# Kernel optimization log

Measured on AMD Instinct MI355X. Metric: run time of the kernel, lower is better.

## Reference

```python
import jax, jax.numpy as jnp
import numpy as np


def setup_inputs() -> dict:
    key = jax.random.key(0)
    k1, k2, k3, k4 = jax.random.split(key, 4)
    B, G, C, T = 4, 40, 13, 1024
    return {
        "x": jax.random.normal(k1, (B, G, C, T), dtype=jnp.float32),
        "query_w": jax.random.normal(k2, (C, C), dtype=jnp.float32),
        "key_w": jax.random.normal(k3, (C, C), dtype=jnp.float32),
        "value_w": jax.random.normal(k4, (C, C), dtype=jnp.float32),
    }


def reference(x, query_w, key_w, value_w):
    # x: [B, 40, 13, T] real -> rfft over time -> [B, 40, 13, F] complex
    x_fft = jnp.fft.rfft(x, axis=-1)
    cdt = x_fft.dtype
    wq = query_w.astype(cdt)  # [13,13] complex (zero imag), shared across the 40 groups
    wk = key_w.astype(cdt)
    wv = value_w.astype(cdt)
    xt = jnp.swapaxes(x_fft, -1, -2)  # [B, 40, F, 13]
    q = xt @ wq                       # [B, 40, F, 13]
    k = xt @ wk
    v = xt @ wv
    scores = jnp.abs(q @ jnp.swapaxes(k, -1, -2))     # [B, 40, F, F] real
    attn = jax.nn.softmax(scores, axis=-1).astype(cdt)
    out = (attn @ v)                                   # [B, 40, F, 13]
    out = jnp.swapaxes(out, -1, -2)                    # [B, 40, 13, F]
    return jnp.fft.irfft(out, axis=-1)                 # [B, 40, 13, 2*(F-1)]
```

## Files before the change

### kernel.cpp

```cpp
#include <hip/hip_runtime.h>
#include <math.h>

#define BDIM 4
#define GDIM 40
#define CDIM 13
#define TDIM 1024
#define FDIM 513
#define BG   (BDIM*GDIM)
#define NROW (BG*FDIM)
#define NCHUNK 9
#define TK 64

typedef _Float16 half4 __attribute__((ext_vector_type(4)));
typedef _Float16 half8 __attribute__((ext_vector_type(8)));
typedef float    f32x4 __attribute__((ext_vector_type(4)));

#define MFMA16(a, b, c) __builtin_amdgcn_mfma_f32_16x16x16f16((a), (b), (c), 0, 0, 0)

__device__ __forceinline__ unsigned bitrev10(unsigned x) { return __brev(x) >> 22; }

__global__ void fft_fwd2(const float* __restrict__ x, float2* __restrict__ xf) {
    __shared__ float re[1024], im[1024];
    const int s2 = blockIdx.x;
    const float* x1 = x + (size_t)(2 * s2) * TDIM;
    const float* x2 = x1 + TDIM;
    for (int t = threadIdx.x; t < 1024; t += blockDim.x) {
        unsigned r = bitrev10(t);
        re[r] = x1[t];
        im[r] = x2[t];
    }
    __syncthreads();
    for (int s = 0; s < 10; ++s) {
        int half = 1 << s;
        for (int j = threadIdx.x; j < 512; j += blockDim.x) {
            int grp = j >> s;
            int pos = j & (half - 1);
            int i1 = (grp << (s + 1)) + pos;
            int i2 = i1 + half;
            float ang = -(float)M_PI * (float)pos / (float)half;
            float sw, cw; __sincosf(ang, &sw, &cw);
            float xr = re[i2], xi = im[i2];
            float tr = cw * xr - sw * xi;
            float ti = cw * xi + sw * xr;
            float ur = re[i1], ui = im[i1];
            re[i1] = ur + tr; im[i1] = ui + ti;
            re[i2] = ur - tr; im[i2] = ui - ti;
        }
        __syncthreads();
    }
    const int sigA = 2 * s2, sigB = sigA + 1;
    const int bgA = sigA / CDIM, cA = sigA % CDIM;
    const int bgB = sigB / CDIM, cB = sigB % CDIM;
    for (int f = threadIdx.x; f < FDIM; f += blockDim.x) {
        int fr = (1024 - f) & 1023;
        float zr = re[f], zi = im[f];
        float wr = re[fr], wi = im[fr];
        xf[((size_t)bgA * FDIM + f) * CDIM + cA] =
            make_float2(0.5f * (zr + wr), 0.5f * (zi - wi));
        xf[((size_t)bgB * FDIM + f) * CDIM + cB] =
            make_float2(0.5f * (zi + wi), 0.5f * (wr - zr));
    }
}

__global__ void qkv_kernel(const float2* __restrict__ xf,
                           const float* __restrict__ wq,
                           const float* __restrict__ wk,
                           const float* __restrict__ wv,
                           float2* __restrict__ q,
                           _Float16* __restrict__ KP,
                           _Float16* __restrict__ VT) {
    int gid = blockIdx.x * blockDim.x + threadIdx.x;
    if (gid >= NROW * CDIM) return;
    int r = gid / CDIM;
    int i = gid - r * CDIM;
    const float2* xrow = xf + (size_t)r * CDIM;
    float qr = 0, qi = 0, kr = 0, ki = 0, vr = 0, vi = 0;
#pragma unroll
    for (int c = 0; c < CDIM; ++c) {
        float2 xc = xrow[c];
        float a = wq[c * CDIM + i]; qr += xc.x * a; qi += xc.y * a;
        float b = wk[c * CDIM + i]; kr += xc.x * b; ki += xc.y * b;
        float d = wv[c * CDIM + i]; vr += xc.x * d; vi += xc.y * d;
    }
    q[gid] = make_float2(qr, qi);

    _Float16* krow = KP + (size_t)r * 64;
    _Float16 h0 = (_Float16)kr;
    _Float16 h1 = (_Float16)ki;
    krow[i]      = h0;
    krow[13 + i] = h1;
    krow[32 + i] = (_Float16)(kr - (float)h0);
    krow[45 + i] = (_Float16)(ki - (float)h1);
    if (i == 12) {
        *(unsigned int*)(krow + 26) = 0u;
        *(unsigned int*)(krow + 28) = 0u;
        *(unsigned int*)(krow + 30) = 0u;
        *(unsigned int*)(krow + 58) = 0u;
        *(unsigned int*)(krow + 60) = 0u;
        *(unsigned int*)(krow + 62) = 0u;
    }
    int bg = r / FDIM;
    int f  = r - bg * FDIM;
    VT[((size_t)(bg * 2 + 0) * 16 + i) * 520 + f] = (_Float16)vr;
    VT[((size_t)(bg * 2 + 1) * 16 + i) * 520 + f] = (_Float16)vi;
}

__global__ __launch_bounds__(256, 4) void attn_kernel(const float2* __restrict__ q,
                                                      const _Float16* __restrict__ KP,
                                                      const _Float16* __restrict__ VT,
                                                      float2* __restrict__ outspec) {
    __shared__ __align__(16) _Float16 Klds[TK * 64];
    __shared__ __align__(16) _Float16 VTlds[2 * 16 * 72];

    const int bg    = blockIdx.x / NCHUNK;
    const int chunk = blockIdx.x % NCHUNK;
    const int tid   = threadIdx.x;
    const int w     = tid >> 6;
    const int lane  = tid & 63;
    const int qlane = lane & 15;
    const int g     = lane >> 4;
    const int frow  = chunk * 64 + w * 16 + qlane;
    const bool writer = (frow < FDIM);
    const int f     = writer ? frow : (FDIM - 1);
    const size_t rowbase = (size_t)(bg * FDIM + f) * CDIM;

    half4 uh[2], ul[2], u2h[2], u2l[2];
#pragma unroll
    for (int c01 = 0; c01 < 2; ++c01) {
#pragma unroll
        for (int j = 0; j < 4; ++j) {
            int k = c01 * 16 + 4 * g + j;
            float a = 0.f, b = 0.f;
            if (k < CDIM) {
                float2 t = q[rowbase + k];          a = t.x;  b = t.y;
            } else if (k < 2 * CDIM) {
                float2 t = q[rowbase + (k - CDIM)]; a = -t.y; b = t.x;
            }
            _Float16 ah = (_Float16)a;
            uh[c01][j]  = ah;
            ul[c01][j]  = (_Float16)(a - (float)ah);
            _Float16 bh = (_Float16)b;
            u2h[c01][j] = bh;
            u2l[c01][j] = (_Float16)(b - (float)bh);
        }
    }

    f32x4 o_re = {0.f, 0.f, 0.f, 0.f};
    f32x4 o_im = {0.f, 0.f, 0.f, 0.f};
    float m = -INFINITY, l = 0.f;

    const _Float16* __restrict__ KPg = KP + (size_t)bg * FDIM * 64;
    const _Float16* __restrict__ VTg = VT + (size_t)bg * 2 * 16 * 520;

    for (int t0 = 0; t0 < FDIM; t0 += TK) {
        __syncthreads();
#pragma unroll
        for (int hh = 0; hh < 2; ++hh) {
            int gr  = tid + hh * 256;
            int krw = gr >> 3, gg = gr & 7;
            half8 val;
#pragma unroll
            for (int e = 0; e < 8; ++e) val[e] = (_Float16)0.f;
            int grow = t0 + krw;
            if (grow < FDIM)
                val = *(const half8*)(KPg + (size_t)grow * 64 + gg * 8);
            *(half8*)(Klds + krw * 64 + ((gg ^ (krw & 7)) << 3)) = val;
        }
        {
            int gk = tid & 7, cc = (tid >> 3) & 15, part = tid >> 7;
            int rb = t0 + gk * 8;
            half8 val;
#pragma unroll
            for (int e = 0; e < 8; ++e) val[e] = (_Float16)0.f;
            if (rb < FDIM) {
                val = *(const half8*)(VTg + ((size_t)(part * 16 + cc)) * 520 + rb);
                if (rb + 8 > FDIM) {
#pragma unroll
                    for (int e = 0; e < 8; ++e) if (rb + e >= FDIM) val[e] = (_Float16)0.f;
                }
            }
            *(half8*)(VTlds + (part * 16 + cc) * 72 + gk * 8) = val;
        }
        __syncthreads();

#pragma unroll
        for (int sub = 0; sub < 4; ++sub) {
            const int arow = sub * 16 + qlane;
            const int rx   = arow & 7;
            const _Float16* kr = Klds + arow * 64;
#define KFRAG(h) (*(const half4*)(kr + (((((h) >> 3)) ^ rx) << 3) + ((h) & 7)))
            half4 wh0 = KFRAG(4 * g);
            half4 wh1 = KFRAG(16 + 4 * g);
            half4 wl0 = KFRAG(32 + 4 * g);
            half4 wl1 = KFRAG(48 + 4 * g);
#undef KFRAG
            f32x4 sre = {0.f, 0.f, 0.f, 0.f};
            f32x4 sim = {0.f, 0.f, 0.f, 0.f};
            sre = MFMA16(wh0, uh[0], sre);
            sre = MFMA16(wh1, uh[1], sre);
            sre = MFMA16(wl0, uh[0], sre);
            sre = MFMA16(wl1, uh[1], sre);
            sre = MFMA16(wh0, ul[0], sre);
            sre = MFMA16(wh1, ul[1], sre);
            sre = MFMA16(wl0, ul[0], sre);
            sre = MFMA16(wl1, ul[1], sre);
            sim = MFMA16(wh0, u2h[0], sim);
            sim = MFMA16(wh1, u2h[1], sim);
            sim = MFMA16(wl0, u2h[0], sim);
            sim = MFMA16(wl1, u2h[1], sim);
            sim = MFMA16(wh0, u2l[0], sim);
            sim = MFMA16(wh1, u2l[1], sim);
            sim = MFMA16(wl0, u2l[0], sim);
            sim = MFMA16(wl1, u2l[1], sim);

            float s0 = sqrtf(fmaf(sre[0], sre[0], sim[0] * sim[0]));
            float s1 = sqrtf(fmaf(sre[1], sre[1], sim[1] * sim[1]));
            float s2 = sqrtf(fmaf(sre[2], sre[2], sim[2] * sim[2]));
            float s3 = sqrtf(fmaf(sre[3], sre[3], sim[3] * sim[3]));
            float tmax = fmaxf(fmaxf(s0, s1), fmaxf(s2, s3));
            tmax = fmaxf(tmax, __shfl_xor(tmax, 16));
            tmax = fmaxf(tmax, __shfl_xor(tmax, 32));
            float mnew  = fmaxf(m, tmax);
            float alpha = __expf(m - mnew);
            m = mnew;
            l *= alpha;
            o_re *= alpha;
            o_im *= alpha;
            float p0 = __expf(s0 - m);
            float p1 = __expf(s1 - m);
            float p2 = __expf(s2 - m);
            float p3 = __expf(s3 - m);
            l += (p0 + p1) + (p2 + p3);
            half4 pk;
            pk[0] = (_Float16)p0; pk[1] = (_Float16)p1;
            pk[2] = (_Float16)p2; pk[3] = (_Float16)p3;

            const int voff = sub * 16 + 4 * g;
            half4 vfr = *(const half4*)(VTlds + qlane * 72 + voff);
            half4 vfi = *(const half4*)(VTlds + (16 + qlane) * 72 + voff);
            o_re = MFMA16(vfr, pk, o_re);
            o_im = MFMA16(vfi, pk, o_im);
        }
    }

    l += __shfl_xor(l, 16);
    l += __shfl_xor(l, 32);
    if (writer) {
        float inv = 1.f / l;
#pragma unroll
        for (int j = 0; j < 4; ++j) {
            int c = 4 * g + j;
            if (c < CDIM)
                outspec[((size_t)(bg * CDIM + c)) * FDIM + frow] =
                    make_float2(o_re[j] * inv, o_im[j] * inv);
        }
    }
}

__global__ void fft_inv2(const float2* __restrict__ spec, float* __restrict__ out) {
    __shared__ float re[1024], im[1024];
    const int s2 = blockIdx.x;
    const float2* Y1 = spec + (size_t)(2 * s2) * FDIM;
    const float2* Y2 = Y1 + FDIM;
    for (int t = threadIdx.x; t < 1024; t += blockDim.x) {
        float a, b, c, d;
        if (t <= 512) {
            float2 y1 = Y1[t], y2 = Y2[t];
            bool edge = (t == 0) | (t == 512);
            a = y1.x; b = edge ? 0.f : y1.y;
            c = y2.x; d = edge ? 0.f : y2.y;
        } else {
            float2 y1 = Y1[1024 - t], y2 = Y2[1024 - t];
            a = y1.x; b = -y1.y;
            c = y2.x; d = -y2.y;
        }
        unsigned r = bitrev10(t);
        re[r] = a - d;
        im[r] = b + c;
    }
    __syncthreads();
    for (int s = 0; s < 10; ++s) {
        int half = 1 << s;
        for (int j = threadIdx.x; j < 512; j += blockDim.x) {
            int grp = j >> s;
            int pos = j & (half - 1);
            int i1 = (grp << (s + 1)) + pos;
            int i2 = i1 + half;
            float ang = (float)M_PI * (float)pos / (float)half;
            float sw, cw; __sincosf(ang, &sw, &cw);
            float xr = re[i2], xi = im[i2];
            float tr = cw * xr - sw * xi;
            float ti = cw * xi + sw * xr;
            float ur = re[i1], ui = im[i1];
            re[i1] = ur + tr; im[i1] = ui + ti;
            re[i2] = ur - tr; im[i2] = ui - ti;
        }
        __syncthreads();
    }
    const float scale = 1.0f / 1024.0f;
    float* o1 = out + (size_t)(2 * s2) * TDIM;
    for (int t = threadIdx.x; t < 1024; t += blockDim.x) {
        o1[t]        = re[t] * scale;
        o1[TDIM + t] = im[t] * scale;
    }
}

extern "C" void kernel_launch(void* const* d_in, const int* in_sizes, int n_in,
                              void* d_out, int out_size, void* d_ws, size_t ws_size,
                              hipStream_t stream) {
    const float* x  = (const float*)d_in[0];
    const float* wq = (const float*)d_in[1];
    const float* wk = (const float*)d_in[2];
    const float* wv = (const float*)d_in[3];
    float* out = (float*)d_out;

    const size_t n = (size_t)NROW * CDIM;
    float2* xf = (float2*)d_ws;
    float2* q  = xf + n;
    _Float16* KP = (_Float16*)(q + n);
    _Float16* VT = KP + (size_t)NROW * 64;

    fft_fwd2<<<BG * CDIM / 2, 256, 0, stream>>>(x, xf);
    qkv_kernel<<<(NROW * CDIM + 255) / 256, 256, 0, stream>>>(xf, wq, wk, wv, q, KP, VT);
    attn_kernel<<<BG * NCHUNK, 256, 0, stream>>>(q, KP, VT, xf );
    fft_inv2<<<BG * CDIM / 2, 256, 0, stream>>>(xf, out);
}
```

Measured before the change: 194.3 us.

## Read K/V fragments directly from global, use 16x16x32 MFMA and lazy softmax rescale

The attention kernel no longer stages K and V tiles through LDS with block barriers. Each wave now loads its MFMA fragments straight from global memory, relying on cache. Score computation switches to the 16x16x32 f16 MFMA, halving the instruction count. Softmax moves to exp2 with log2e folded into Q, and the running-max rescale is skipped unless the max grows by more than 8. Block order is swapped so chunks of the same bg run together for cache reuse, and the FFT kernels launch with 512 threads. The trade-off is more redundant global/L2 traffic in exchange for no LDS synchronization, with some risk to fp16 range from the delayed rescale.

```diff
diff --git a/kernel.cpp b/kernel.cpp
--- a/kernel.cpp
+++ b/kernel.cpp
@@ -9,13 +9,13 @@
 #define BG   (BDIM*GDIM)
 #define NROW (BG*FDIM)
 #define NCHUNK 9
-#define TK 64
 
 typedef _Float16 half4 __attribute__((ext_vector_type(4)));
 typedef _Float16 half8 __attribute__((ext_vector_type(8)));
 typedef float    f32x4 __attribute__((ext_vector_type(4)));
 
 #define MFMA16(a, b, c) __builtin_amdgcn_mfma_f32_16x16x16f16((a), (b), (c), 0, 0, 0)
+#define MFMA32(a, b, c) __builtin_amdgcn_mfma_f32_16x16x32_f16((a), (b), (c), 0, 0, 0)
 
 __device__ __forceinline__ unsigned bitrev10(unsigned x) { return __brev(x) >> 22; }
 
@@ -105,15 +105,58 @@
     VT[((size_t)(bg * 2 + 1) * 16 + i) * 520 + f] = (_Float16)vi;
 }
 
+__device__ __forceinline__ void attn_step(
+    half4 a0, half4 a1, half4 a2, half4 a3, half4 vfr, half4 vfi,
+    const half8& Quh, const half8& Qul, const half8& Qu2h, const half8& Qu2l,
+    f32x4& ore, f32x4& oim, float& m, float& l)
+{
+    half8 whh, wll;
+#pragma unroll
+    for (int j = 0; j < 4; ++j) {
+        whh[j] = a0[j]; whh[4 + j] = a1[j];
+        wll[j] = a2[j]; wll[4 + j] = a3[j];
+    }
+    f32x4 sre = {0.f, 0.f, 0.f, 0.f};
+    f32x4 sim = {0.f, 0.f, 0.f, 0.f};
+    sre = MFMA32(whh, Quh, sre);
+    sre = MFMA32(wll, Quh, sre);
+    sre = MFMA32(whh, Qul, sre);
+    sre = MFMA32(wll, Qul, sre);
+    sim = MFMA32(whh, Qu2h, sim);
+    sim = MFMA32(wll, Qu2h, sim);
+    sim = MFMA32(whh, Qu2l, sim);
+    sim = MFMA32(wll, Qu2l, sim);
+    float s0 = sqrtf(fmaf(sre[0], sre[0], sim[0] * sim[0]));
+    float s1 = sqrtf(fmaf(sre[1], sre[1], sim[1] * sim[1]));
+    float s2 = sqrtf(fmaf(sre[2], sre[2], sim[2] * sim[2]));
+    float s3 = sqrtf(fmaf(sre[3], sre[3], sim[3] * sim[3]));
+    float tm = fmaxf(fmaxf(s0, s1), fmaxf(s2, s3));
+    tm = fmaxf(tm, __shfl_xor(tm, 16));
+    tm = fmaxf(tm, __shfl_xor(tm, 32));
+    if (!__all(tm <= m + 8.f)) {
+        float mnew  = fmaxf(m, tm);
+        float alpha = exp2f(m - mnew);
+        l *= alpha; ore *= alpha; oim *= alpha;
+        m = mnew;
+    }
+    float p0 = exp2f(s0 - m);
+    float p1 = exp2f(s1 - m);
+    float p2 = exp2f(s2 - m);
+    float p3 = exp2f(s3 - m);
+    l += (p0 + p1) + (p2 + p3);
+    half4 pk;
+    pk[0] = (_Float16)p0; pk[1] = (_Float16)p1;
+    pk[2] = (_Float16)p2; pk[3] = (_Float16)p3;
+    ore = MFMA16(vfr, pk, ore);
+    oim = MFMA16(vfi, pk, oim);
+}
+
 __global__ __launch_bounds__(256, 4) void attn_kernel(const float2* __restrict__ q,
                                                       const _Float16* __restrict__ KP,
                                                       const _Float16* __restrict__ VT,
                                                       float2* __restrict__ outspec) {
-    __shared__ __align__(16) _Float16 Klds[TK * 64];
-    __shared__ __align__(16) _Float16 VTlds[2 * 16 * 72];
-
-    const int bg    = blockIdx.x / NCHUNK;
-    const int chunk = blockIdx.x % NCHUNK;
+    const int bg    = blockIdx.x % BG;
+    const int chunk = blockIdx.x / BG;
     const int tid   = threadIdx.x;
     const int w     = tid >> 6;
     const int lane  = tid & 63;
@@ -122,137 +165,85 @@
     const int frow  = chunk * 64 + w * 16 + qlane;
     const bool writer = (frow < FDIM);
     const int f     = writer ? frow : (FDIM - 1);
-    const size_t rowbase = (size_t)(bg * FDIM + f) * CDIM;
-
-    half4 uh[2], ul[2], u2h[2], u2l[2];
-#pragma unroll
-    for (int c01 = 0; c01 < 2; ++c01) {
+    const size_t rowbase = ((size_t)bg * FDIM + f) * CDIM;
+
+    const float LOG2E = 1.44269504088896340736f;
+    half8 Quh, Qul, Qu2h, Qu2l;
+#pragma unroll
+    for (int c = 0; c < 2; ++c) {
 #pragma unroll
         for (int j = 0; j < 4; ++j) {
-            int k = c01 * 16 + 4 * g + j;
+            const int e = 4 * c + j;
+            const int k = 16 * c + 4 * g + j;
             float a = 0.f, b = 0.f;
             if (k < CDIM) {
                 float2 t = q[rowbase + k];          a = t.x;  b = t.y;
             } else if (k < 2 * CDIM) {
                 float2 t = q[rowbase + (k - CDIM)]; a = -t.y; b = t.x;
             }
+            a *= LOG2E;
+            b *= LOG2E;
             _Float16 ah = (_Float16)a;
-            uh[c01][j]  = ah;
-            ul[c01][j]  = (_Float16)(a - (float)ah);
+            Quh[e]  = ah;
+            Qul[e]  = (_Float16)(a - (float)ah);
             _Float16 bh = (_Float16)b;
-            u2h[c01][j] = bh;
-            u2l[c01][j] = (_Float16)(b - (float)bh);
-        }
-    }
-
-    f32x4 o_re = {0.f, 0.f, 0.f, 0.f};
-    f32x4 o_im = {0.f, 0.f, 0.f, 0.f};
+            Qu2h[e] = bh;
+            Qu2l[e] = (_Float16)(b - (float)bh);
+        }
+    }
+
+    f32x4 ore = {0.f, 0.f, 0.f, 0.f};
+    f32x4 oim = {0.f, 0.f, 0.f, 0.f};
     float m = -INFINITY, l = 0.f;
 
     const _Float16* __restrict__ KPg = KP + (size_t)bg * FDIM * 64;
     const _Float16* __restrict__ VTg = VT + (size_t)bg * 2 * 16 * 520;
 
-    for (int t0 = 0; t0 < FDIM; t0 += TK) {
-        __syncthreads();
-#pragma unroll
-        for (int hh = 0; hh < 2; ++hh) {
-            int gr  = tid + hh * 256;
-            int krw = gr >> 3, gg = gr & 7;
-            half8 val;
-#pragma unroll
-            for (int e = 0; e < 8; ++e) val[e] = (_Float16)0.f;
-            int grow = t0 + krw;
-            if (grow < FDIM)
-                val = *(const half8*)(KPg + (size_t)grow * 64 + gg * 8);
-            *(half8*)(Klds + krw * 64 + ((gg ^ (krw & 7)) << 3)) = val;
-        }
-        {
-            int gk = tid & 7, cc = (tid >> 3) & 15, part = tid >> 7;
-            int rb = t0 + gk * 8;
-            half8 val;
-#pragma unroll
-            for (int e = 0; e < 8; ++e) val[e] = (_Float16)0.f;
-            if (rb < FDIM) {
-                val = *(const half8*)(VTg + ((size_t)(part * 16 + cc)) * 520 + rb);
-                if (rb + 8 > FDIM) {
-#pragma unroll
-                    for (int e = 0; e < 8; ++e) if (rb + e >= FDIM) val[e] = (_Float16)0.f;
-                }
-            }
-            *(half8*)(VTlds + (part * 16 + cc) * 72 + gk * 8) = val;
-        }
-        __syncthreads();
-
+    for (int t = 0; t < 8; ++t) {
 #pragma unroll
         for (int sub = 0; sub < 4; ++sub) {
-            const int arow = sub * 16 + qlane;
-            const int rx   = arow & 7;
-            const _Float16* kr = Klds + arow * 64;
-#define KFRAG(h) (*(const half4*)(kr + (((((h) >> 3)) ^ rx) << 3) + ((h) & 7)))
-            half4 wh0 = KFRAG(4 * g);
-            half4 wh1 = KFRAG(16 + 4 * g);
-            half4 wl0 = KFRAG(32 + 4 * g);
-            half4 wl1 = KFRAG(48 + 4 * g);
-#undef KFRAG
-            f32x4 sre = {0.f, 0.f, 0.f, 0.f};
-            f32x4 sim = {0.f, 0.f, 0.f, 0.f};
-            sre = MFMA16(wh0, uh[0], sre);
-            sre = MFMA16(wh1, uh[1], sre);
-            sre = MFMA16(wl0, uh[0], sre);
-            sre = MFMA16(wl1, uh[1], sre);
-            sre = MFMA16(wh0, ul[0], sre);
-            sre = MFMA16(wh1, ul[1], sre);
-            sre = MFMA16(wl0, ul[0], sre);
-            sre = MFMA16(wl1, ul[1], sre);
-            sim = MFMA16(wh0, u2h[0], sim);
-            sim = MFMA16(wh1, u2h[1], sim);
-            sim = MFMA16(wl0, u2h[0], sim);
-            sim = MFMA16(wl1, u2h[1], sim);
-            sim = MFMA16(wh0, u2l[0], sim);
-            sim = MFMA16(wh1, u2l[1], sim);
-            sim = MFMA16(wl0, u2l[0], sim);
-            sim = MFMA16(wl1, u2l[1], sim);
-
-            float s0 = sqrtf(fmaf(sre[0], sre[0], sim[0] * sim[0]));
-            float s1 = sqrtf(fmaf(sre[1], sre[1], sim[1] * sim[1]));
-            float s2 = sqrtf(fmaf(sre[2], sre[2], sim[2] * sim[2]));
-            float s3 = sqrtf(fmaf(sre[3], sre[3], sim[3] * sim[3]));
-            float tmax = fmaxf(fmaxf(s0, s1), fmaxf(s2, s3));
-            tmax = fmaxf(tmax, __shfl_xor(tmax, 16));
-            tmax = fmaxf(tmax, __shfl_xor(tmax, 32));
-            float mnew  = fmaxf(m, tmax);
-            float alpha = __expf(m - mnew);
-            m = mnew;
-            l *= alpha;
-            o_re *= alpha;
-            o_im *= alpha;
-            float p0 = __expf(s0 - m);
-            float p1 = __expf(s1 - m);
-            float p2 = __expf(s2 - m);
-            float p3 = __expf(s3 - m);
-            l += (p0 + p1) + (p2 + p3);
-            half4 pk;
-            pk[0] = (_Float16)p0; pk[1] = (_Float16)p1;
-            pk[2] = (_Float16)p2; pk[3] = (_Float16)p3;
-
-            const int voff = sub * 16 + 4 * g;
-            half4 vfr = *(const half4*)(VTlds + qlane * 72 + voff);
-            half4 vfi = *(const half4*)(VTlds + (16 + qlane) * 72 + voff);
-            o_re = MFMA16(vfr, pk, o_re);
-            o_im = MFMA16(vfi, pk, o_im);
-        }
-    }
-
-    l += __shfl_xor(l, 16);
-    l += __shfl_xor(l, 32);
+            const int arow = t * 64 + sub * 16 + qlane;
+            const _Float16* kr = KPg + arow * 64 + 4 * g;
+            half4 a0 = *(const half4*)(kr);
+            half4 a1 = *(const half4*)(kr + 16);
+            half4 a2 = *(const half4*)(kr + 32);
+            half4 a3 = *(const half4*)(kr + 48);
+            const int f0 = t * 64 + sub * 16 + 4 * g;
+            half4 vfr = *(const half4*)(VTg + qlane * 520 + f0);
+            half4 vfi = *(const half4*)(VTg + (16 + qlane) * 520 + f0);
+            attn_step(a0, a1, a2, a3, vfr, vfi,
+                      Quh, Qul, Qu2h, Qu2l, ore, oim, m, l);
+        }
+    }
+    {
+        half4 z = {};
+        half4 a0 = z, a1 = z, a2 = z, a3 = z, vfr = z, vfi = z;
+        if (qlane == 0) {
+            const _Float16* kr = KPg + 512 * 64 + 4 * g;
+            a0 = *(const half4*)(kr);
+            a1 = *(const half4*)(kr + 16);
+            a2 = *(const half4*)(kr + 32);
+            a3 = *(const half4*)(kr + 48);
+        }
+        if (g == 0) {
+            vfr[0] = VTg[qlane * 520 + 512];
+            vfi[0] = VTg[(16 + qlane) * 520 + 512];
+        }
+        attn_step(a0, a1, a2, a3, vfr, vfi,
+                  Quh, Qul, Qu2h, Qu2l, ore, oim, m, l);
+    }
+
+    float lt = l;
+    lt += __shfl_xor(lt, 16);
+    lt += __shfl_xor(lt, 32);
     if (writer) {
-        float inv = 1.f / l;
+        float inv = 1.f / lt;
 #pragma unroll
         for (int j = 0; j < 4; ++j) {
             int c = 4 * g + j;
             if (c < CDIM)
                 outspec[((size_t)(bg * CDIM + c)) * FDIM + frow] =
-                    make_float2(o_re[j] * inv, o_im[j] * inv);
+                    make_float2(ore[j] * inv, oim[j] * inv);
         }
     }
 }
@@ -320,8 +311,8 @@
     _Float16* KP = (_Float16*)(q + n);
     _Float16* VT = KP + (size_t)NROW * 64;
 
-    fft_fwd2<<<BG * CDIM / 2, 256, 0, stream>>>(x, xf);
+    fft_fwd2<<<BG * CDIM / 2, 512, 0, stream>>>(x, xf);
     qkv_kernel<<<(NROW * CDIM + 255) / 256, 256, 0, stream>>>(xf, wq, wk, wv, q, KP, VT);
     attn_kernel<<<BG * NCHUNK, 256, 0, stream>>>(q, KP, VT, xf );
-    fft_inv2<<<BG * CDIM / 2, 256, 0, stream>>>(xf, out);
-}
+    fft_inv2<<<BG * CDIM / 2, 512, 0, stream>>>(xf, out);
+}
```

After: 231.4 us. 19.1% more time.
